# Kernel optimization log

Measured on AMD Instinct MI355X. Metric: run time of the kernel, lower is better.

The kernel has to match this reference:

```python
import jax, jax.numpy as jnp
import numpy as np

N_GENE, N_DRUG, N_CLASS, N_FAM = 100000, 50000, 2000, 5000
D = 64
E_CG, E_CP, E_GF = 2000000, 100000, 200000
N_PAIRS = 100000


def setup_inputs() -> dict:
    key = jax.random.key(0)
    ks = jax.random.split(key, 32)
    nrm = lambda k, s, sc=0.1: jax.random.normal(k, s, jnp.float32) * sc
    ri = lambda k, n, hi: jax.random.randint(k, (n,), 0, hi, jnp.int32)
    inp = {
        "gene_emb": nrm(ks[0], (N_GENE, D)),
        "drug_emb": nrm(ks[1], (N_DRUG, D)),
        "class_emb": nrm(ks[2], (N_CLASS, D)),
        "family_emb": nrm(ks[3], (N_FAM, D)),
        "W_msg": nrm(ks[4], (2, 6, D, D)),
        "b_msg": jnp.zeros((2, 6, D), jnp.float32),
        "W_root": nrm(ks[5], (2, 6, D, D)),
        "Wc1": nrm(ks[6], (2 * D, D)),
        "bc1": jnp.zeros((D,), jnp.float32),
        "Wc2": nrm(ks[7], (D, 4)),
        "bc2": jnp.zeros((4,), jnp.float32),
        "e_cg_src": ri(ks[8], E_CG, N_DRUG), "e_cg_dst": ri(ks[9], E_CG, N_GENE),
        "e_gc_src": ri(ks[10], E_CG, N_GENE), "e_gc_dst": ri(ks[11], E_CG, N_DRUG),
        "e_cp_src": ri(ks[12], E_CP, N_DRUG), "e_cp_dst": ri(ks[13], E_CP, N_CLASS),
        "e_pc_src": ri(ks[14], E_CP, N_CLASS), "e_pc_dst": ri(ks[15], E_CP, N_DRUG),
        "e_gf_src": ri(ks[16], E_GF, N_GENE), "e_gf_dst": ri(ks[17], E_GF, N_FAM),
        "e_fg_src": ri(ks[18], E_GF, N_FAM), "e_fg_dst": ri(ks[19], E_GF, N_GENE),
        "pair_drug": ri(ks[20], N_PAIRS, N_DRUG),
        "pair_gene": ri(ks[21], N_PAIRS, N_GENE),
    }
    return inp


def _sage(x_src, x_dst, src, dst, n_dst, Wm, bm, Wr):
    # PyG SAGEConv(aggr='mean'): lin_l(mean_j x_src[j]) + lin_r(x_dst)
    msg = x_src[src]                                            # [E, D] gather
    agg = jax.ops.segment_sum(msg, dst, num_segments=n_dst)     # [n_dst, D]
    cnt = jax.ops.segment_sum(jnp.ones(src.shape, msg.dtype), dst, num_segments=n_dst)
    mean = agg / jnp.maximum(cnt, 1.0)[:, None]                 # isolated nodes -> 0
    return mean @ Wm + bm + x_dst @ Wr


def reference(gene_emb, drug_emb, class_emb, family_emb, W_msg, b_msg, W_root,
              Wc1, bc1, Wc2, bc2,
              e_cg_src, e_cg_dst, e_gc_src, e_gc_dst, e_cp_src, e_cp_dst,
              e_pc_src, e_pc_dst, e_gf_src, e_gf_dst, e_fg_src, e_fg_dst,
              pair_drug, pair_gene):
    sizes = {"gene": N_GENE, "compound": N_DRUG, "pclass": N_CLASS, "family": N_FAM}
    rels = [  # (src_type, dst_type, src_idx, dst_idx), order matches W_msg relation axis
        ("compound", "gene", e_cg_src, e_cg_dst),
        ("gene", "compound", e_gc_src, e_gc_dst),
        ("compound", "pclass", e_cp_src, e_cp_dst),
        ("pclass", "compound", e_pc_src, e_pc_dst),
        ("gene", "family", e_gf_src, e_gf_dst),
        ("family", "gene", e_fg_src, e_fg_dst),
    ]
    x = {"gene": gene_emb, "compound": drug_emb, "pclass": class_emb, "family": family_emb}
    num_layers = 2
    for l in range(num_layers):
        out = {k: jnp.zeros((sizes[k], D), jnp.float32) for k in sizes}  # HeteroConv aggr='sum'
        for r, (s, d, src, dst) in enumerate(rels):
            out[d] = out[d] + _sage(x[s], x[d], src, dst, sizes[d],
                                    W_msg[l, r], b_msg[l, r], W_root[l, r])
        x = out
        if l < num_layers - 1:
            x = {k: jax.nn.relu(v) for k, v in x.items()}  # dropout = identity (eval)
    h = jnp.concatenate([x["compound"][pair_drug], x["gene"][pair_gene]], axis=-1)  # [N, 2D]
    h = jax.nn.relu(h @ Wc1 + bc1)
    return h @ Wc2 + bc2  # [N, 4]
```

## Files before the change

### kernel.cpp

```cpp
#include <hip/hip_runtime.h>
#include <hip/hip_bf16.h>

#define NG 100000
#define ND 50000
#define NC 2000
#define NF 5000
#define DD 64

#define BSH 9
#define BINW 512
#define NREL 6
#define NB_CG ((NG + BINW - 1) / BINW)
#define NB_GC ((ND + BINW - 1) / BINW)
#define NB_CP ((NC + BINW - 1) / BINW)
#define NB_PC ((ND + BINW - 1) / BINW)
#define NB_GF ((NF + BINW - 1) / BINW)
#define NB_FG ((NG + BINW - 1) / BINW)
#define TOTB (NB_CG + NB_GC + NB_CP + NB_PC + NB_GF + NB_FG)
#define CHUNK 4096

typedef _Float16 h2_t __attribute__((ext_vector_type(2)));
typedef _Float16 half8 __attribute__((ext_vector_type(8)));
typedef float f32x4 __attribute__((ext_vector_type(4)));

__device__ inline uint packh2_rne(float a, float b) {
    h2_t h; h.x = (_Float16)a; h.y = (_Float16)b;
    return __builtin_bit_cast(uint, h);
}
__device__ inline uint packh2(float a, float b) {
    return __builtin_bit_cast(uint, __builtin_amdgcn_cvt_pkrtz(a, b));
}
__device__ inline float2 h2f2(uint u) {
    h2_t h = __builtin_bit_cast(h2_t, u);
    return make_float2((float)h.x, (float)h.y);
}
__device__ inline float fdot2u(uint m, uint w, float acc) {
#if __has_builtin(__builtin_amdgcn_fdot2)
    return __builtin_amdgcn_fdot2(__builtin_bit_cast(h2_t, m),
                                  __builtin_bit_cast(h2_t, w), acc, false);
#else
    float2 a = h2f2(m), b = h2f2(w);
    return acc + a.x * b.x + a.y * b.y;
#endif
}

struct Cvt4 { const float* in[4]; uint* out[4]; int n2[4]; };
struct EdgeJobs {
    const int* src[NREL]; const int* dst[NREL];
    int binbase[NREL]; int E[NREL]; int blk_end[NREL];
};
struct BPackJobs {
    const float* A[6]; const float* B[6]; const float* Ra[6]; const float* Rb[6];
    uint4* out[6]; int nkt[6];
};

struct MegaA {
    EdgeJobs ej; Cvt4 cv; BPackJobs bp;
    const float* Wc1; uint2* pwWc1;
    int hist_blocks, cvt_blocks;
    int* ghist;
};
__global__ __launch_bounds__(256) void megaA_kernel(MegaA a) {
    int b = blockIdx.x;
    if (b < a.hist_blocks) {
        __shared__ int lh[TOTB];
        for (int t = threadIdx.x; t < TOTB; t += 256) lh[t] = 0;
        __syncthreads();
        int j = 0;
        while (b >= a.ej.blk_end[j]) ++j;
        int b0 = j ? a.ej.blk_end[j - 1] : 0;
        int e0 = (b - b0) * CHUNK;
        const int* dst = a.ej.dst[j];
        int E = a.ej.E[j], bb = a.ej.binbase[j];
        for (int t = threadIdx.x; t < CHUNK; t += 256) {
            int e = e0 + t;
            if (e < E) atomicAdd(&lh[bb + (dst[e] >> BSH)], 1);
        }
        __syncthreads();
        for (int t = threadIdx.x; t < TOTB; t += 256)
            if (lh[t]) atomicAdd(&a.ghist[t], lh[t]);
    } else if (b < a.hist_blocks + a.cvt_blocks) {
        int cb = b - a.hist_blocks;
        for (int j = 0; j < 4; ++j) {
            int n2 = a.cv.n2[j];
            const float2* ip = (const float2*)a.cv.in[j];
            uint* op = a.cv.out[j];
            for (int i = cb * 256 + threadIdx.x; i < n2; i += a.cvt_blocks * 256)
                op[i] = packh2_rne(ip[i].x, ip[i].y);
        }
    } else if (b == a.hist_blocks + a.cvt_blocks) {
        const float* A = a.Wc1;
        uint2* o = a.pwWc1;
        for (int t = threadIdx.x; t < 32 * 64; t += 256) {
            int k4 = t >> 6, c = t & 63;
            float v0 = A[(4 * k4 + 0) * 64 + c];
            float v1 = A[(4 * k4 + 1) * 64 + c];
            float v2 = A[(4 * k4 + 2) * 64 + c];
            float v3 = A[(4 * k4 + 3) * 64 + c];
            o[t] = make_uint2(packh2_rne(v0, v1), packh2_rne(v2, v3));
        }
    } else {
        int pj = b - a.hist_blocks - a.cvt_blocks - 1;
        const float* A = a.bp.A[pj];
        const float* B = a.bp.B[pj];
        const float* Ra = a.bp.Ra[pj];
        const float* Rb = a.bp.Rb[pj];
        uint4* o = a.bp.out[pj];
        int n = a.bp.nkt[pj] * 4 * 64;
        for (int t = threadIdx.x; t < n; t += 256) {
            int kt = t >> 8, nt = (t >> 6) & 3, l = t & 63;
            int col = nt * 16 + (l & 15);
            float v[8];
#pragma unroll
            for (int j = 0; j < 8; ++j) {
                int k = kt * 32 + ((l >> 4) << 3) + j;
                int sel = k >> 6, r = k & 63;
                float x;
                if (sel == 0) x = A[r * 64 + col];
                else if (sel == 1 && B) x = B[r * 64 + col];
                else x = Ra[r * 64 + col] + (Rb ? Rb[r * 64 + col] : 0.f);
                v[j] = x;
            }
            o[t] = make_uint4(packh2_rne(v[0], v[1]), packh2_rne(v[2], v[3]),
                              packh2_rne(v[4], v[5]), packh2_rne(v[6], v[7]));
        }
    }
}

__global__ void scanB_kernel(const int* __restrict__ ghist, int* __restrict__ gbinstart,
                             int* __restrict__ gcursor) {
    int lane = threadIdx.x;
    if (lane >= 64) return;
    int carry = 0;
    for (int base = 0; base < TOTB; base += 64) {
        int idx = base + lane;
        int v = (idx < TOTB) ? ghist[idx] : 0;
        int ts = v;
        for (int d = 1; d < 64; d <<= 1) { int t = __shfl_up(ts, d); if (lane >= d) ts += t; }
        int excl = carry + ts - v;
        if (idx < TOTB) { gbinstart[idx] = excl; gcursor[idx] = excl; }
        carry += __shfl(ts, 63);
    }
    if (lane == 0) gbinstart[TOTB] = carry;
}

__global__ __launch_bounds__(256) void scatC_kernel(EdgeJobs ej, int* __restrict__ gcursor,
                                                    int* __restrict__ binned) {
    __shared__ int lh[TOTB], lbase[TOTB];
    for (int t = threadIdx.x; t < TOTB; t += 256) lh[t] = 0;
    __syncthreads();
    int b = blockIdx.x, j = 0;
    while (b >= ej.blk_end[j]) ++j;
    int b0 = j ? ej.blk_end[j - 1] : 0;
    int e0 = (b - b0) * CHUNK;
    const int* dst = ej.dst[j];
    const int* srcp = ej.src[j];
    int E = ej.E[j], bb = ej.binbase[j];
    for (int t = threadIdx.x; t < CHUNK; t += 256) {
        int e = e0 + t;
        if (e < E) atomicAdd(&lh[bb + (dst[e] >> BSH)], 1);
    }
    __syncthreads();
    for (int t = threadIdx.x; t < TOTB; t += 256) {
        int c = lh[t];
        if (c) { lbase[t] = atomicAdd(&gcursor[t], c); lh[t] = 0; }
    }
    __syncthreads();
    for (int t = threadIdx.x; t < CHUNK; t += 256) {
        int e = e0 + t;
        if (e < E) {
            int d = dst[e];
            int bin = bb + (d >> BSH);
            int p = atomicAdd(&lh[bin], 1);
            binned[lbase[bin] + p] = (srcp[e] << BSH) | (d & (BINW - 1));
        }
    }
}

struct BinMeta { int relbase[NREL + 1]; int* off[NREL]; int ndst[NREL]; };
__global__ __launch_bounds__(256) void csrD_kernel(BinMeta bmt, const int* __restrict__ gbinstart,
                                                   const int* __restrict__ binned,
                                                   int* __restrict__ adj) {
    __shared__ int lcnt[BINW], lexc[BINW];
    int b = blockIdx.x, j = 0;
    while (b >= bmt.relbase[j + 1]) ++j;
    int lb = b - bmt.relbase[j];
    int n0 = lb << BSH;
    int nn = bmt.ndst[j] - n0; if (nn > BINW) nn = BINW;
    int es = gbinstart[b], ee = gbinstart[b + 1];
    for (int t = threadIdx.x; t < BINW; t += 256) lcnt[t] = 0;
    __syncthreads();
    for (int t = es + threadIdx.x; t < ee; t += 256)
        atomicAdd(&lcnt[binned[t] & (BINW - 1)], 1);
    __syncthreads();
    if (threadIdx.x < 64) {
        int lane = threadIdx.x, carry = 0;
        for (int base = 0; base < BINW; base += 64) {
            int v = lcnt[base + lane];
            int ts = v;
            for (int d = 1; d < 64; d <<= 1) { int t2 = __shfl_up(ts, d); if (lane >= d) ts += t2; }
            lexc[base + lane] = carry + ts - v;
            carry += __shfl(ts, 63);
        }
    }
    __syncthreads();
    int* off = bmt.off[j];
    for (int t = threadIdx.x; t < nn; t += 256) off[n0 + t] = es + lexc[t];
    if (threadIdx.x == 0 && n0 + nn == bmt.ndst[j]) off[bmt.ndst[j]] = ee;
    for (int t = threadIdx.x; t < BINW; t += 256) lcnt[t] = 0;
    __syncthreads();
    for (int t = es + threadIdx.x; t < ee; t += 256) {
        int v = binned[t];
        int dl = v & (BINW - 1);
        int p = atomicAdd(&lcnt[dl], 1);
        adj[es + lexc[dl] + p] = v >> BSH;
    }
}

__device__ inline void gather2(const int* __restrict__ off, const int* __restrict__ adj,
                               const uint2* __restrict__ xp,
                               int ia, bool hb, int rg, int cq,
                               float4& ma, float4& mb) {
    int a0 = off[ia], a1 = off[ia + 1];
    int b1v = hb ? off[ia + 2] : a1;
    int na = a1 - a0, nb = b1v - a1;
    const int* Ba = adj + a0;
    const int* Bb = adj + a1;
    float4 sa = {0.f, 0.f, 0.f, 0.f}, sb = {0.f, 0.f, 0.f, 0.f};
    int mx = na > nb ? na : nb;
    if (mx <= 8) {
        for (int j = 0; j < mx; j += 4) {
            int e = j + rg;
            if (j < na) {
                int l = na - 1;
                int s0 = Ba[e < l ? e : l];
                uint2 v0 = xp[(long long)s0 * 16 + cq];
                if (e < na) { float2 lo = h2f2(v0.x), hi = h2f2(v0.y); sa.x += lo.x; sa.y += lo.y; sa.z += hi.x; sa.w += hi.y; }
            }
            if (j < nb) {
                int l = nb - 1;
                int s0 = Bb[e < l ? e : l];
                uint2 v0 = xp[(long long)s0 * 16 + cq];
                if (e < nb) { float2 lo = h2f2(v0.x), hi = h2f2(v0.y); sb.x += lo.x; sb.y += lo.y; sb.z += hi.x; sb.w += hi.y; }
            }
        }
    } else {
        for (int j = 0; j < mx; j += 16) {
            int e0 = j + rg, e1 = j + 4 + rg, e2 = j + 8 + rg, e3 = j + 12 + rg;
            if (j < na) {
                int l = na - 1;
                int s0 = Ba[e0 < l ? e0 : l], s1 = Ba[e1 < l ? e1 : l];
                int s2 = Ba[e2 < l ? e2 : l], s3 = Ba[e3 < l ? e3 : l];
                uint2 v0 = xp[(long long)s0 * 16 + cq];
                uint2 v1 = xp[(long long)s1 * 16 + cq];
                uint2 v2 = xp[(long long)s2 * 16 + cq];
                uint2 v3 = xp[(long long)s3 * 16 + cq];
                if (e0 < na) { float2 lo = h2f2(v0.x), hi = h2f2(v0.y); sa.x += lo.x; sa.y += lo.y; sa.z += hi.x; sa.w += hi.y; }
                if (e1 < na) { float2 lo = h2f2(v1.x), hi = h2f2(v1.y); sa.x += lo.x; sa.y += lo.y; sa.z += hi.x; sa.w += hi.y; }
                if (e2 < na) { float2 lo = h2f2(v2.x), hi = h2f2(v2.y); sa.x += lo.x; sa.y += lo.y; sa.z += hi.x; sa.w += hi.y; }
                if (e3 < na) { float2 lo = h2f2(v3.x), hi = h2f2(v3.y); sa.x += lo.x; sa.y += lo.y; sa.z += hi.x; sa.w += hi.y; }
            }
            if (j < nb) {
                int l = nb - 1;
                int s0 = Bb[e0 < l ? e0 : l], s1 = Bb[e1 < l ? e1 : l];
                int s2 = Bb[e2 < l ? e2 : l], s3 = Bb[e3 < l ? e3 : l];
                uint2 v0 = xp[(long long)s0 * 16 + cq];
                uint2 v1 = xp[(long long)s1 * 16 + cq];
                uint2 v2 = xp[(long long)s2 * 16 + cq];
                uint2 v3 = xp[(long long)s3 * 16 + cq];
                if (e0 < nb) { float2 lo = h2f2(v0.x), hi = h2f2(v0.y); sb.x += lo.x; sb.y += lo.y; sb.z += hi.x; sb.w += hi.y; }
                if (e1 < nb) { float2 lo = h2f2(v1.x), hi = h2f2(v1.y); sb.x += lo.x; sb.y += lo.y; sb.z += hi.x; sb.w += hi.y; }
                if (e2 < nb) { float2 lo = h2f2(v2.x), hi = h2f2(v2.y); sb.x += lo.x; sb.y += lo.y; sb.z += hi.x; sb.w += hi.y; }
                if (e3 < nb) { float2 lo = h2f2(v3.x), hi = h2f2(v3.y); sb.x += lo.x; sb.y += lo.y; sb.z += hi.x; sb.w += hi.y; }
            }
        }
    }
    sa.x += __shfl_xor(sa.x, 16); sa.y += __shfl_xor(sa.y, 16);
    sa.z += __shfl_xor(sa.z, 16); sa.w += __shfl_xor(sa.w, 16);
    sa.x += __shfl_xor(sa.x, 32); sa.y += __shfl_xor(sa.y, 32);
    sa.z += __shfl_xor(sa.z, 32); sa.w += __shfl_xor(sa.w, 32);
    sb.x += __shfl_xor(sb.x, 16); sb.y += __shfl_xor(sb.y, 16);
    sb.z += __shfl_xor(sb.z, 16); sb.w += __shfl_xor(sb.w, 16);
    sb.x += __shfl_xor(sb.x, 32); sb.y += __shfl_xor(sb.y, 32);
    sb.z += __shfl_xor(sb.z, 32); sb.w += __shfl_xor(sb.w, 32);
    float inva = 1.f / fmaxf((float)na, 1.f);
    float invb = 1.f / fmaxf((float)nb, 1.f);
    ma.x = sa.x * inva; ma.y = sa.y * inva; ma.z = sa.z * inva; ma.w = sa.w * inva;
    mb.x = sb.x * invb; mb.y = sb.y * invb; mb.z = sb.z * invb; mb.w = sb.w * invb;
}

struct GatherJobs {
    const int* offA[4]; const int* offB[4];
    const uint2* xA[4]; const uint2* xB[4];
    uint2* cat[4]; int cstr[4]; int n[4]; int hasB[4]; int blk_end[4];
};
__global__ __launch_bounds__(256) void gather_kernel(GatherJobs g, const int* __restrict__ adj,
                                                     int njobs) {
    int b = blockIdx.x, j = 0;
    while (b >= g.blk_end[j]) ++j;
    int b0 = j ? g.blk_end[j - 1] : 0;
    int jb = g.blk_end[j] - b0;
    int n = g.n[j], cstr = g.cstr[j], hasB = g.hasB[j];
    const int* offA = g.offA[j];
    const int* offB = g.offB[j];
    const uint2* xA = g.xA[j];
    const uint2* xB = g.xB[j];
    uint2* cat = g.cat[j];
    int tid = threadIdx.x;
    int w = tid >> 6, lane = tid & 63, rg = lane >> 4, cq = lane & 15;
    for (int i0 = (b - b0) * 8; i0 < n; i0 += jb * 8) {
        int ia = i0 + w * 2;
        if (ia >= n) continue;
        int ib = ia + 1;
        bool hb = (ib < n);
        float4 mA0, mA1;
        gather2(offA, adj, xA, ia, hb, rg, cq, mA0, mA1);
        if (rg == 0) {
            cat[(long long)ia * cstr + cq] = make_uint2(packh2(mA0.x, mA0.y), packh2(mA0.z, mA0.w));
            if (hb) cat[(long long)ib * cstr + cq] = make_uint2(packh2(mA1.x, mA1.y), packh2(mA1.z, mA1.w));
        }
        if (hasB) {
            float4 mB0, mB1;
            gather2(offB, adj, xB, ia, hb, rg, cq, mB0, mB1);
            if (rg == 0) {
                cat[(long long)ia * cstr + 16 + cq] = make_uint2(packh2(mB0.x, mB0.y), packh2(mB0.z, mB0.w));
                if (hb) cat[(long long)ib * cstr + 16 + cq] = make_uint2(packh2(mB1.x, mB1.y), packh2(mB1.z, mB1.w));
            }
        }
    }
}

struct ApplyJobs {
    const uint4* cat[4]; const uint4* xr[4]; const uint4* Bimg[4];
    const float* bA[4]; const float* bB[4];
    ushort* out[4];
    int cat_kt[4]; int cstr4[4]; int n[4]; int relu[4]; int blk_end[4];
};
__global__ __launch_bounds__(256) void apply_kernel(ApplyJobs a, int njobs) {
    int b = blockIdx.x, j = 0;
    while (b >= a.blk_end[j]) ++j;
    int b0 = j ? a.blk_end[j - 1] : 0;
    int jb = a.blk_end[j] - b0;
    int n = a.n[j], cat_kt = a.cat_kt[j], cstr4 = a.cstr4[j], relu = a.relu[j];
    int K_kt = cat_kt + 2;
    const uint4* cat = a.cat[j];
    const uint4* xr = a.xr[j];
    const uint4* Bimg = a.Bimg[j];
    const float* bA = a.bA[j];
    const float* bB = a.bB[j];
    ushort* out = a.out[j];
    int tid = threadIdx.x;
    int w = tid >> 6, lane = tid & 63;
    int mrow = lane & 15, koct = lane >> 4;
    int tiles = (n + 15) >> 4;
    for (int t = (b - b0) * 4 + w; t < tiles; t += jb * 4) {
        int m0 = t << 4;
        int row = m0 + mrow;
        if (row > n - 1) row = n - 1;
        f32x4 acc0 = {0.f, 0.f, 0.f, 0.f};
        f32x4 acc1 = {0.f, 0.f, 0.f, 0.f};
        f32x4 acc2 = {0.f, 0.f, 0.f, 0.f};
        f32x4 acc3 = {0.f, 0.f, 0.f, 0.f};
        for (int kt = 0; kt < K_kt; ++kt) {
            uint4 av;
            if (kt < cat_kt) av = cat[(long long)row * cstr4 + kt * 4 + koct];
            else av = xr[(long long)row * 8 + (kt - cat_kt) * 4 + koct];
            half8 af = __builtin_bit_cast(half8, av);
            const uint4* bp = Bimg + kt * 256 + lane;
            half8 b0f = __builtin_bit_cast(half8, bp[0]);
            half8 b1f = __builtin_bit_cast(half8, bp[64]);
            half8 b2f = __builtin_bit_cast(half8, bp[128]);
            half8 b3f = __builtin_bit_cast(half8, bp[192]);
            acc0 = __builtin_amdgcn_mfma_f32_16x16x32_f16(af, b0f, acc0, 0, 0, 0);
            acc1 = __builtin_amdgcn_mfma_f32_16x16x32_f16(af, b1f, acc1, 0, 0, 0);
            acc2 = __builtin_amdgcn_mfma_f32_16x16x32_f16(af, b2f, acc2, 0, 0, 0);
            acc3 = __builtin_amdgcn_mfma_f32_16x16x32_f16(af, b3f, acc3, 0, 0, 0);
        }
        int c = lane & 15, r0 = m0 + (lane >> 4) * 4;
        f32x4 accs[4] = {acc0, acc1, acc2, acc3};
#pragma unroll
        for (int nt = 0; nt < 4; ++nt) {
            int col = nt * 16 + c;
            float bias = bA[col] + (bB ? bB[col] : 0.f);
#pragma unroll
            for (int r = 0; r < 4; ++r) {
                int rw = r0 + r;
                if (rw < n) {
                    float v = accs[nt][r] + bias;
                    if (relu) v = fmaxf(v, 0.f);
                    out[(long long)rw * 64 + col] = __builtin_bit_cast(ushort, (_Float16)v);
                }
            }
        }
    }
}

__global__ __launch_bounds__(256) void classifier_kernel(
        const ushort* __restrict__ xc, const ushort* __restrict__ xg,
        const int* __restrict__ pd, const int* __restrict__ pg,
        const uint2* __restrict__ gW1, const float* __restrict__ bc1,
        const float* __restrict__ Wc2, const float* __restrict__ bc2,
        float* __restrict__ out, int n) {
    __shared__ uint2 sW1[2048];
    __shared__ float sW2[256];
    __shared__ uint2 shp[4][32];
    __shared__ float sh1[4][65];
    int tid = threadIdx.x;
    for (int t = tid; t < 2048; t += 256) sW1[t] = gW1[t];
    if (tid < 256) sW2[tid] = Wc2[tid];
    __syncthreads();
    int lane = tid & 63, sub = tid >> 6;
    float b1 = bc1[lane];
    const uint* xcp = (const uint*)xc;
    const uint* xgp = (const uint*)xg;
    for (int base = blockIdx.x * 4; base < n; base += gridDim.x * 4) {
        int p = base + sub;
        if (p >= n) continue;
        int dp = pd[p], gp = pg[p];
        uint v = (lane < 32) ? xcp[(long long)dp * 32 + lane]
                             : xgp[(long long)gp * 32 + (lane - 32)];
        ((uint*)&shp[sub][0])[lane] = v;
        float acc = b1;
#pragma unroll
        for (int k4 = 0; k4 < 32; ++k4) {
            uint2 wv = sW1[k4 * 64 + lane];
            uint2 mv = shp[sub][k4];
            acc = fdot2u(mv.x, wv.x, acc);
            acc = fdot2u(mv.y, wv.y, acc);
        }
        sh1[sub][lane] = fmaxf(acc, 0.f);
        if (lane < 4) {
            float a2 = bc2[lane];
#pragma unroll 16
            for (int k = 0; k < 64; ++k) a2 += sh1[sub][k] * sW2[k * 4 + lane];
            out[(long long)p * 4 + lane] = a2;
        }
    }
}

extern "C" void kernel_launch(void* const* d_in, const int* in_sizes, int n_in,
                              void* d_out, int out_size, void* d_ws, size_t ws_size,
                              hipStream_t stream) {
    const float* gene = (const float*)d_in[0];
    const float* drug = (const float*)d_in[1];
    const float* pcls = (const float*)d_in[2];
    const float* famb = (const float*)d_in[3];
    const float* Wm   = (const float*)d_in[4];
    const float* bm   = (const float*)d_in[5];
    const float* Wr   = (const float*)d_in[6];
    const float* Wc1  = (const float*)d_in[7];
    const float* bc1  = (const float*)d_in[8];
    const float* Wc2  = (const float*)d_in[9];
    const float* bc2  = (const float*)d_in[10];
    const int* ecg_s = (const int*)d_in[11];
    const int* ecg_d = (const int*)d_in[12];
    const int* egc_s = (const int*)d_in[13];
    const int* egc_d = (const int*)d_in[14];
    const int* ecp_s = (const int*)d_in[15];
    const int* ecp_d = (const int*)d_in[16];
    const int* epc_s = (const int*)d_in[17];
    const int* epc_d = (const int*)d_in[18];
    const int* egf_s = (const int*)d_in[19];
    const int* egf_d = (const int*)d_in[20];
    const int* efg_s = (const int*)d_in[21];
    const int* efg_d = (const int*)d_in[22];
    const int* pair_d = (const int*)d_in[23];
    const int* pair_g = (const int*)d_in[24];
    const int E_CG = in_sizes[11];
    const int E_CP = in_sizes[15];
    const int E_GF = in_sizes[19];
    const int N_PAIRS = in_sizes[23];
    const long long TOT_E = 2LL * E_CG + 2LL * E_CP + 2LL * E_GF;

    ushort* g16   = (ushort*)d_ws;
    ushort* d16   = g16   + (long long)NG * DD;
    ushort* p16   = d16   + (long long)ND * DD;
    ushort* f16b  = p16   + (long long)NC * DD;
    ushort* x1g16 = f16b  + (long long)NF * DD;
    ushort* x1c16 = x1g16 + (long long)NG * DD;
    ushort* x1p16 = x1c16 + (long long)ND * DD;
    ushort* x1f16 = x1p16 + (long long)NC * DD;
    ushort* x2g16 = g16;
    ushort* x2c16 = d16;
    uint2* pwWc1 = (uint2*)(x1f16 + (long long)NF * DD);
    uint4* bimg = (uint4*)(pwWc1 + 2048);
    int* ghist = (int*)(bimg + 6 * 1536);
    int* gbinstart = ghist + TOTB;
    int* gcursor = gbinstart + TOTB + 1;
    int* off_cg = gcursor + TOTB;
    int* off_gc = off_cg + NG + 1;
    int* off_cp = off_gc + ND + 1;
    int* off_pc = off_cp + NC + 1;
    int* off_gf = off_pc + ND + 1;
    int* off_fg = off_gf + NF + 1;
    long long binned_off = (long long)(off_fg + NG + 1 - (int*)d_ws);
    binned_off = (binned_off + 3) & ~3LL;
    int* binned = (int*)d_ws + binned_off;
    int* adj    = binned + TOT_E;
    uint2* cat_c = (uint2*)binned;
    uint2* cat_p = cat_c + (long long)ND * 32;
    uint2* cat_f = cat_p + (long long)NC * 16;
    uint2* cat_g = (uint2*)(adj + TOT_E);

    auto WmLR = [&](int l, int r) { return Wm + (long long)(l * 6 + r) * DD * DD; };
    auto WrLR = [&](int l, int r) { return Wr + (long long)(l * 6 + r) * DD * DD; };
    auto bmLR = [&](int l, int r) { return bm + (long long)(l * 6 + r) * DD; };

    EdgeJobs ej;
    const int* srcs[NREL] = {ecg_s, egc_s, ecp_s, epc_s, egf_s, efg_s};
    const int* dsts[NREL] = {ecg_d, egc_d, ecp_d, epc_d, egf_d, efg_d};
    int Es[NREL] = {E_CG, E_CG, E_CP, E_CP, E_GF, E_GF};
    int bb[NREL] = {0, NB_CG, NB_CG + NB_GC, NB_CG + NB_GC + NB_CP,
                    NB_CG + NB_GC + NB_CP + NB_PC, NB_CG + NB_GC + NB_CP + NB_PC + NB_GF};
    int acc_blocks = 0;
    for (int j = 0; j < NREL; ++j) {
        ej.src[j] = srcs[j]; ej.dst[j] = dsts[j];
        ej.E[j] = Es[j]; ej.binbase[j] = bb[j];
        acc_blocks += (Es[j] + CHUNK - 1) / CHUNK;
        ej.blk_end[j] = acc_blocks;
    }
    const int THIST = acc_blocks;
    const int CVTB = 1024;

    hipMemsetAsync(ghist, 0, TOTB * sizeof(int), stream);
    MegaA ma;
    ma.ej = ej;
    ma.cv.in[0] = gene; ma.cv.out[0] = (uint*)g16;  ma.cv.n2[0] = NG * DD / 2;
    ma.cv.in[1] = drug; ma.cv.out[1] = (uint*)d16;  ma.cv.n2[1] = ND * DD / 2;
    ma.cv.in[2] = pcls; ma.cv.out[2] = (uint*)p16;  ma.cv.n2[2] = NC * DD / 2;
    ma.cv.in[3] = famb; ma.cv.out[3] = (uint*)f16b; ma.cv.n2[3] = NF * DD / 2;
    ma.Wc1 = Wc1; ma.pwWc1 = pwWc1;
    auto setbp = [&](int j, const float* A, const float* B, const float* Ra, const float* Rb, int nkt) {
        ma.bp.A[j] = A; ma.bp.B[j] = B; ma.bp.Ra[j] = Ra; ma.bp.Rb[j] = Rb;
        ma.bp.out[j] = bimg + j * 1536; ma.bp.nkt[j] = nkt;
    };
    setbp(0, WmLR(0, 0), WmLR(0, 5), WrLR(0, 0), WrLR(0, 5), 6);
    setbp(1, WmLR(0, 1), WmLR(0, 3), WrLR(0, 1), WrLR(0, 3), 6);
    setbp(2, WmLR(0, 2), nullptr,    WrLR(0, 2), nullptr,    4);
    setbp(3, WmLR(0, 4), nullptr,    WrLR(0, 4), nullptr,    4);
    setbp(4, WmLR(1, 0), WmLR(1, 5), WrLR(1, 0), WrLR(1, 5), 6);
    setbp(5, WmLR(1, 1), WmLR(1, 3), WrLR(1, 1), WrLR(1, 3), 6);
    ma.hist_blocks = THIST; ma.cvt_blocks = CVTB;
    ma.ghist = ghist;
    megaA_kernel<<<THIST + CVTB + 1 + 6, 256, 0, stream>>>(ma);

    scanB_kernel<<<1, 64, 0, stream>>>(ghist, gbinstart, gcursor);
    scatC_kernel<<<THIST, 256, 0, stream>>>(ej, gcursor, binned);
    BinMeta bmt;
    int rb[NREL + 1] = {0, NB_CG, NB_CG + NB_GC, NB_CG + NB_GC + NB_CP,
                        NB_CG + NB_GC + NB_CP + NB_PC,
                        NB_CG + NB_GC + NB_CP + NB_PC + NB_GF, TOTB};
    int* offs[NREL] = {off_cg, off_gc, off_cp, off_pc, off_gf, off_fg};
    int nds[NREL] = {NG, ND, NC, ND, NF, NG};
    for (int j = 0; j <= NREL; ++j) bmt.relbase[j] = rb[j];
    for (int j = 0; j < NREL; ++j) { bmt.off[j] = offs[j]; bmt.ndst[j] = nds[j]; }
    csrD_kernel<<<TOTB, 256, 0, stream>>>(bmt, gbinstart, binned, adj);

    auto gblk = [](int n) { int b = (n + 7) / 8; return b > 2048 ? 2048 : b; };
    auto ablk = [](int n) { int b = ((n + 15) / 16 + 3) / 4; return b > 1024 ? 1024 : b; };

    {
        GatherJobs g;
        auto setg = [&](int j, const int* oA, const uint2* xA, const int* oB, const uint2* xB,
                        uint2* cat, int cstr, int n, int hb) {
            g.offA[j] = oA; g.offB[j] = oB; g.xA[j] = xA; g.xB[j] = xB;
            g.cat[j] = cat; g.cstr[j] = cstr; g.n[j] = n; g.hasB[j] = hb;
        };
        setg(0, off_cg, (const uint2*)d16, off_fg, (const uint2*)f16b, cat_g, 32, NG, 1);
        setg(1, off_gc, (const uint2*)g16, off_pc, (const uint2*)p16, cat_c, 32, ND, 1);
        setg(2, off_cp, (const uint2*)d16, nullptr, nullptr, cat_p, 16, NC, 0);
        setg(3, off_gf, (const uint2*)g16, nullptr, nullptr, cat_f, 16, NF, 0);
        int acc = 0;
        for (int j = 0; j < 4; ++j) { acc += gblk(g.n[j]); g.blk_end[j] = acc; }
        gather_kernel<<<acc, 256, 0, stream>>>(g, adj, 4);

        ApplyJobs ap;
        auto seta = [&](int j, const uint2* cat, int ckt, int cstr4, const ushort* xr,
                        const uint4* Bi, const float* biA, const float* biB,
                        ushort* out, int n, int relu) {
            ap.cat[j] = (const uint4*)cat; ap.cat_kt[j] = ckt; ap.cstr4[j] = cstr4;
            ap.xr[j] = (const uint4*)xr; ap.Bimg[j] = Bi; ap.bA[j] = biA; ap.bB[j] = biB;
            ap.out[j] = out; ap.n[j] = n; ap.relu[j] = relu;
        };
        seta(0, cat_g, 4, 16, g16,  bimg + 0 * 1536, bmLR(0, 0), bmLR(0, 5), x1g16, NG, 1);
        seta(1, cat_c, 4, 16, d16,  bimg + 1 * 1536, bmLR(0, 1), bmLR(0, 3), x1c16, ND, 1);
        seta(2, cat_p, 2, 8,  p16,  bimg + 2 * 1536, bmLR(0, 2), nullptr,    x1p16, NC, 1);
        seta(3, cat_f, 2, 8,  f16b, bimg + 3 * 1536, bmLR(0, 4), nullptr,    x1f16, NF, 1);
        int acc2 = 0;
        for (int j = 0; j < 4; ++j) { acc2 += ablk(ap.n[j]); ap.blk_end[j] = acc2; }
        apply_kernel<<<acc2, 256, 0, stream>>>(ap, 4);
    }

    {
        GatherJobs g;
        g.offA[0] = off_cg; g.offB[0] = off_fg;
        g.xA[0] = (const uint2*)x1c16; g.xB[0] = (const uint2*)x1f16;
        g.cat[0] = cat_g; g.cstr[0] = 32; g.n[0] = NG; g.hasB[0] = 1;
        g.offA[1] = off_gc; g.offB[1] = off_pc;
        g.xA[1] = (const uint2*)x1g16; g.xB[1] = (const uint2*)x1p16;
        g.cat[1] = cat_c; g.cstr[1] = 32; g.n[1] = ND; g.hasB[1] = 1;
        for (int j = 2; j < 4; ++j) { g.offA[j] = nullptr; g.offB[j] = nullptr; g.xA[j] = nullptr; g.xB[j] = nullptr; g.cat[j] = nullptr; g.cstr[j] = 16; g.n[j] = 0; g.hasB[j] = 0; }
        int acc = gblk(NG); g.blk_end[0] = acc; acc += gblk(ND); g.blk_end[1] = acc;
        g.blk_end[2] = acc; g.blk_end[3] = acc;
        gather_kernel<<<acc, 256, 0, stream>>>(g, adj, 2);

        ApplyJobs ap;
        ap.cat[0] = (const uint4*)cat_g; ap.cat_kt[0] = 4; ap.cstr4[0] = 16;
        ap.xr[0] = (const uint4*)x1g16; ap.Bimg[0] = bimg + 4 * 1536;
        ap.bA[0] = bmLR(1, 0); ap.bB[0] = bmLR(1, 5);
        ap.out[0] = x2g16; ap.n[0] = NG; ap.relu[0] = 0;
        ap.cat[1] = (const uint4*)cat_c; ap.cat_kt[1] = 4; ap.cstr4[1] = 16;
        ap.xr[1] = (const uint4*)x1c16; ap.Bimg[1] = bimg + 5 * 1536;
        ap.bA[1] = bmLR(1, 1); ap.bB[1] = bmLR(1, 3);
        ap.out[1] = x2c16; ap.n[1] = ND; ap.relu[1] = 0;
        for (int j = 2; j < 4; ++j) { ap.cat[j] = nullptr; ap.xr[j] = nullptr; ap.Bimg[j] = nullptr; ap.bA[j] = nullptr; ap.bB[j] = nullptr; ap.out[j] = nullptr; ap.n[j] = 0; ap.relu[j] = 0; ap.cat_kt[j] = 2; ap.cstr4[j] = 8; }
        int acc2 = ablk(NG); ap.blk_end[0] = acc2; acc2 += ablk(ND); ap.blk_end[1] = acc2;
        ap.blk_end[2] = acc2; ap.blk_end[3] = acc2;
        apply_kernel<<<acc2, 256, 0, stream>>>(ap, 2);
    }

    int cblocks = (N_PAIRS + 3) / 4;
    if (cblocks > 2048) cblocks = 2048;
    classifier_kernel<<<cblocks, 256, 0, stream>>>(x2c16, x2g16, pair_d, pair_g,
                                                   pwWc1, bc1, Wc2, bc2,
                                                   (float*)d_out, N_PAIRS);
}
```

Baseline: 473.4 us.

## Restructure gather into per-relation jobs with 16-byte fp16 loads and packed-half accumulation

Replaces the paired-relation gather with six independent per-relation jobs. Each job gets a block count proportional to its edge count and writes its own column half of the concat buffer. Each lane now loads 16 bytes (half8) per row instead of 8 bytes and accumulates in packed fp16 rather than fp32. Low-degree relations use a one-node-per-8-lanes mode so short neighbour lists are not spread across a whole wave. The intent is fewer load instructions, better bandwidth use and better load balance. The cost is reduced accumulation precision: fp16 sums over high-degree nodes may lose accuracy or overflow.

```diff
diff --git a/kernel.cpp b/kernel.cpp
--- a/kernel.cpp
+++ b/kernel.cpp
@@ -26,9 +26,6 @@
 __device__ inline uint packh2_rne(float a, float b) {
     h2_t h; h.x = (_Float16)a; h.y = (_Float16)b;
     return __builtin_bit_cast(uint, h);
-}
-__device__ inline uint packh2(float a, float b) {
-    return __builtin_bit_cast(uint, __builtin_amdgcn_cvt_pkrtz(a, b));
 }
 __device__ inline float2 h2f2(uint u) {
     h2_t h = __builtin_bit_cast(h2_t, u);
@@ -217,115 +214,74 @@
     }
 }
 
-__device__ inline void gather2(const int* __restrict__ off, const int* __restrict__ adj,
-                               const uint2* __restrict__ xp,
-                               int ia, bool hb, int rg, int cq,
-                               float4& ma, float4& mb) {
-    int a0 = off[ia], a1 = off[ia + 1];
-    int b1v = hb ? off[ia + 2] : a1;
-    int na = a1 - a0, nb = b1v - a1;
-    const int* Ba = adj + a0;
-    const int* Bb = adj + a1;
-    float4 sa = {0.f, 0.f, 0.f, 0.f}, sb = {0.f, 0.f, 0.f, 0.f};
-    int mx = na > nb ? na : nb;
-    if (mx <= 8) {
-        for (int j = 0; j < mx; j += 4) {
-            int e = j + rg;
-            if (j < na) {
-                int l = na - 1;
-                int s0 = Ba[e < l ? e : l];
-                uint2 v0 = xp[(long long)s0 * 16 + cq];
-                if (e < na) { float2 lo = h2f2(v0.x), hi = h2f2(v0.y); sa.x += lo.x; sa.y += lo.y; sa.z += hi.x; sa.w += hi.y; }
-            }
-            if (j < nb) {
-                int l = nb - 1;
-                int s0 = Bb[e < l ? e : l];
-                uint2 v0 = xp[(long long)s0 * 16 + cq];
-                if (e < nb) { float2 lo = h2f2(v0.x), hi = h2f2(v0.y); sb.x += lo.x; sb.y += lo.y; sb.z += hi.x; sb.w += hi.y; }
-            }
-        }
-    } else {
-        for (int j = 0; j < mx; j += 16) {
-            int e0 = j + rg, e1 = j + 4 + rg, e2 = j + 8 + rg, e3 = j + 12 + rg;
-            if (j < na) {
-                int l = na - 1;
-                int s0 = Ba[e0 < l ? e0 : l], s1 = Ba[e1 < l ? e1 : l];
-                int s2 = Ba[e2 < l ? e2 : l], s3 = Ba[e3 < l ? e3 : l];
-                uint2 v0 = xp[(long long)s0 * 16 + cq];
-                uint2 v1 = xp[(long long)s1 * 16 + cq];
-                uint2 v2 = xp[(long long)s2 * 16 + cq];
-                uint2 v3 = xp[(long long)s3 * 16 + cq];
-                if (e0 < na) { float2 lo = h2f2(v0.x), hi = h2f2(v0.y); sa.x += lo.x; sa.y += lo.y; sa.z += hi.x; sa.w += hi.y; }
-                if (e1 < na) { float2 lo = h2f2(v1.x), hi = h2f2(v1.y); sa.x += lo.x; sa.y += lo.y; sa.z += hi.x; sa.w += hi.y; }
-                if (e2 < na) { float2 lo = h2f2(v2.x), hi = h2f2(v2.y); sa.x += lo.x; sa.y += lo.y; sa.z += hi.x; sa.w += hi.y; }
-                if (e3 < na) { float2 lo = h2f2(v3.x), hi = h2f2(v3.y); sa.x += lo.x; sa.y += lo.y; sa.z += hi.x; sa.w += hi.y; }
-            }
-            if (j < nb) {
-                int l = nb - 1;
-                int s0 = Bb[e0 < l ? e0 : l], s1 = Bb[e1 < l ? e1 : l];
-                int s2 = Bb[e2 < l ? e2 : l], s3 = Bb[e3 < l ? e3 : l];
-                uint2 v0 = xp[(long long)s0 * 16 + cq];
-                uint2 v1 = xp[(long long)s1 * 16 + cq];
-                uint2 v2 = xp[(long long)s2 * 16 + cq];
-                uint2 v3 = xp[(long long)s3 * 16 + cq];
-                if (e0 < nb) { float2 lo = h2f2(v0.x), hi = h2f2(v0.y); sb.x += lo.x; sb.y += lo.y; sb.z += hi.x; sb.w += hi.y; }
-                if (e1 < nb) { float2 lo = h2f2(v1.x), hi = h2f2(v1.y); sb.x += lo.x; sb.y += lo.y; sb.z += hi.x; sb.w += hi.y; }
-                if (e2 < nb) { float2 lo = h2f2(v2.x), hi = h2f2(v2.y); sb.x += lo.x; sb.y += lo.y; sb.z += hi.x; sb.w += hi.y; }
-                if (e3 < nb) { float2 lo = h2f2(v3.x), hi = h2f2(v3.y); sb.x += lo.x; sb.y += lo.y; sb.z += hi.x; sb.w += hi.y; }
-            }
-        }
-    }
-    sa.x += __shfl_xor(sa.x, 16); sa.y += __shfl_xor(sa.y, 16);
-    sa.z += __shfl_xor(sa.z, 16); sa.w += __shfl_xor(sa.w, 16);
-    sa.x += __shfl_xor(sa.x, 32); sa.y += __shfl_xor(sa.y, 32);
-    sa.z += __shfl_xor(sa.z, 32); sa.w += __shfl_xor(sa.w, 32);
-    sb.x += __shfl_xor(sb.x, 16); sb.y += __shfl_xor(sb.y, 16);
-    sb.z += __shfl_xor(sb.z, 16); sb.w += __shfl_xor(sb.w, 16);
-    sb.x += __shfl_xor(sb.x, 32); sb.y += __shfl_xor(sb.y, 32);
-    sb.z += __shfl_xor(sb.z, 32); sb.w += __shfl_xor(sb.w, 32);
-    float inva = 1.f / fmaxf((float)na, 1.f);
-    float invb = 1.f / fmaxf((float)nb, 1.f);
-    ma.x = sa.x * inva; ma.y = sa.y * inva; ma.z = sa.z * inva; ma.w = sa.w * inva;
-    mb.x = sb.x * invb; mb.y = sb.y * invb; mb.z = sb.z * invb; mb.w = sb.w * invb;
-}
-
-struct GatherJobs {
-    const int* offA[4]; const int* offB[4];
-    const uint2* xA[4]; const uint2* xB[4];
-    uint2* cat[4]; int cstr[4]; int n[4]; int hasB[4]; int blk_end[4];
-};
-__global__ __launch_bounds__(256) void gather_kernel(GatherJobs g, const int* __restrict__ adj,
-                                                     int njobs) {
+struct GJob { const int* off; const uint4* x; uint4* cat; int cstr, colbase, n, mode; };
+struct GatherJobs { GJob jb[6]; int blk_end[6]; };
+
+__global__ __launch_bounds__(256) void gather_kernel(GatherJobs g, const int* __restrict__ adj) {
     int b = blockIdx.x, j = 0;
     while (b >= g.blk_end[j]) ++j;
     int b0 = j ? g.blk_end[j - 1] : 0;
-    int jb = g.blk_end[j] - b0;
-    int n = g.n[j], cstr = g.cstr[j], hasB = g.hasB[j];
-    const int* offA = g.offA[j];
-    const int* offB = g.offB[j];
-    const uint2* xA = g.xA[j];
-    const uint2* xB = g.xB[j];
-    uint2* cat = g.cat[j];
-    int tid = threadIdx.x;
-    int w = tid >> 6, lane = tid & 63, rg = lane >> 4, cq = lane & 15;
-    for (int i0 = (b - b0) * 8; i0 < n; i0 += jb * 8) {
-        int ia = i0 + w * 2;
-        if (ia >= n) continue;
-        int ib = ia + 1;
-        bool hb = (ib < n);
-        float4 mA0, mA1;
-        gather2(offA, adj, xA, ia, hb, rg, cq, mA0, mA1);
-        if (rg == 0) {
-            cat[(long long)ia * cstr + cq] = make_uint2(packh2(mA0.x, mA0.y), packh2(mA0.z, mA0.w));
-            if (hb) cat[(long long)ib * cstr + cq] = make_uint2(packh2(mA1.x, mA1.y), packh2(mA1.z, mA1.w));
-        }
-        if (hasB) {
-            float4 mB0, mB1;
-            gather2(offB, adj, xB, ia, hb, rg, cq, mB0, mB1);
-            if (rg == 0) {
-                cat[(long long)ia * cstr + 16 + cq] = make_uint2(packh2(mB0.x, mB0.y), packh2(mB0.z, mB0.w));
-                if (hb) cat[(long long)ib * cstr + 16 + cq] = make_uint2(packh2(mB1.x, mB1.y), packh2(mB1.z, mB1.w));
+    int nbk = g.blk_end[j] - b0;
+    GJob jb = g.jb[j];
+    int tid = threadIdx.x, w = tid >> 6, lane = tid & 63;
+    int cq = lane & 7, rg = lane >> 3;
+    if (jb.mode == 0) {
+        int side = rg >> 2, sub = rg & 3;
+        int npair = (jb.n + 1) >> 1;
+        for (int p = (b - b0) * 4 + w; p < npair; p += nbk * 4) {
+            int ia = p * 2;
+            bool hb = (ia + 1 < jb.n);
+            int a0 = jb.off[ia], a1 = jb.off[ia + 1];
+            int b1 = hb ? jb.off[ia + 2] : a1;
+            int cnt = side ? (b1 - a1) : (a1 - a0);
+            const int* base = adj + (side ? a1 : a0);
+            half8 acc = {0, 0, 0, 0, 0, 0, 0, 0};
+            int full = cnt & ~3;
+            for (int e = sub; e < full; e += 4) {
+                int idx = base[e];
+                acc += *(const half8*)(jb.x + (long long)idx * 8 + cq);
             }
+            int e = full + sub;
+            if (e < cnt) {
+                int idx = base[e];
+                acc += *(const half8*)(jb.x + (long long)idx * 8 + cq);
+            }
+            uint4 u = __builtin_bit_cast(uint4, acc), o;
+            o.x = __shfl_xor((int)u.x, 8); o.y = __shfl_xor((int)u.y, 8);
+            o.z = __shfl_xor((int)u.z, 8); o.w = __shfl_xor((int)u.w, 8);
+            acc += __builtin_bit_cast(half8, o);
+            u = __builtin_bit_cast(uint4, acc);
+            o.x = __shfl_xor((int)u.x, 16); o.y = __shfl_xor((int)u.y, 16);
+            o.z = __shfl_xor((int)u.z, 16); o.w = __shfl_xor((int)u.w, 16);
+            acc += __builtin_bit_cast(half8, o);
+            float invf = 1.f / fmaxf((float)cnt, 1.f);
+            _Float16 ih = (_Float16)invf;
+            half8 iv = {ih, ih, ih, ih, ih, ih, ih, ih};
+            acc *= iv;
+            if (sub == 0 && (side == 0 || hb)) {
+                int node = ia + side;
+                jb.cat[(long long)node * jb.cstr + jb.colbase + cq] =
+                    __builtin_bit_cast(uint4, acc);
+            }
+        }
+    } else {
+        for (int gp = (b - b0) * 4 + w; gp * 8 < jb.n; gp += nbk * 4) {
+            int node = gp * 8 + rg;
+            int nc = node < jb.n ? node : jb.n - 1;
+            int o0 = jb.off[nc], o1 = jb.off[nc + 1];
+            int cnt = (node < jb.n) ? (o1 - o0) : 0;
+            half8 acc = {0, 0, 0, 0, 0, 0, 0, 0};
+            for (int t = 0; t < cnt; ++t) {
+                int idx = adj[o0 + t];
+                acc += *(const half8*)(jb.x + (long long)idx * 8 + cq);
+            }
+            float invf = 1.f / fmaxf((float)cnt, 1.f);
+            _Float16 ih = (_Float16)invf;
+            half8 iv = {ih, ih, ih, ih, ih, ih, ih, ih};
+            acc *= iv;
+            if (node < jb.n)
+                jb.cat[(long long)node * jb.cstr + jb.colbase + cq] =
+                    __builtin_bit_cast(uint4, acc);
         }
     }
 }
@@ -497,10 +453,10 @@
     binned_off = (binned_off + 3) & ~3LL;
     int* binned = (int*)d_ws + binned_off;
     int* adj    = binned + TOT_E;
-    uint2* cat_c = (uint2*)binned;
-    uint2* cat_p = cat_c + (long long)ND * 32;
-    uint2* cat_f = cat_p + (long long)NC * 16;
-    uint2* cat_g = (uint2*)(adj + TOT_E);
+    uint4* cat_c = (uint4*)binned;
+    uint4* cat_p = cat_c + (long long)ND * 16;
+    uint4* cat_f = cat_p + (long long)NC * 8;
+    uint4* cat_g = (uint4*)(adj + TOT_E);
 
     auto WmLR = [&](int l, int r) { return Wm + (long long)(l * 6 + r) * DD * DD; };
     auto WrLR = [&](int l, int r) { return Wr + (long long)(l * 6 + r) * DD * DD; };
@@ -556,29 +512,31 @@
     for (int j = 0; j < NREL; ++j) { bmt.off[j] = offs[j]; bmt.ndst[j] = nds[j]; }
     csrD_kernel<<<TOTB, 256, 0, stream>>>(bmt, gbinstart, binned, adj);
 
-    auto gblk = [](int n) { int b = (n + 7) / 8; return b > 2048 ? 2048 : b; };
     auto ablk = [](int n) { int b = ((n + 15) / 16 + 3) / 4; return b > 1024 ? 1024 : b; };
+    auto gb = [](int E) { int b = E / 1024; if (b < 8) b = 8; if (b > 2048) b = 2048; return b; };
 
     {
         GatherJobs g;
-        auto setg = [&](int j, const int* oA, const uint2* xA, const int* oB, const uint2* xB,
-                        uint2* cat, int cstr, int n, int hb) {
-            g.offA[j] = oA; g.offB[j] = oB; g.xA[j] = xA; g.xB[j] = xB;
-            g.cat[j] = cat; g.cstr[j] = cstr; g.n[j] = n; g.hasB[j] = hb;
+        int acc = 0;
+        auto setg = [&](int j, const int* off, const ushort* x, uint4* cat,
+                        int cstr, int colbase, int n, int mode, int E) {
+            g.jb[j].off = off; g.jb[j].x = (const uint4*)x; g.jb[j].cat = cat;
+            g.jb[j].cstr = cstr; g.jb[j].colbase = colbase; g.jb[j].n = n; g.jb[j].mode = mode;
+            acc += gb(E); g.blk_end[j] = acc;
         };
-        setg(0, off_cg, (const uint2*)d16, off_fg, (const uint2*)f16b, cat_g, 32, NG, 1);
-        setg(1, off_gc, (const uint2*)g16, off_pc, (const uint2*)p16, cat_c, 32, ND, 1);
-        setg(2, off_cp, (const uint2*)d16, nullptr, nullptr, cat_p, 16, NC, 0);
-        setg(3, off_gf, (const uint2*)g16, nullptr, nullptr, cat_f, 16, NF, 0);
-        int acc = 0;
-        for (int j = 0; j < 4; ++j) { acc += gblk(g.n[j]); g.blk_end[j] = acc; }
-        gather_kernel<<<acc, 256, 0, stream>>>(g, adj, 4);
+        setg(0, off_cg, d16,  cat_g, 16, 0, NG, 0, E_CG);
+        setg(1, off_fg, f16b, cat_g, 16, 8, NG, 1, E_GF);
+        setg(2, off_gc, g16,  cat_c, 16, 0, ND, 0, E_CG);
+        setg(3, off_pc, p16,  cat_c, 16, 8, ND, 1, E_CP);
+        setg(4, off_cp, d16,  cat_p, 8, 0, NC, 0, E_CP);
+        setg(5, off_gf, g16,  cat_f, 8, 0, NF, 0, E_GF);
+        gather_kernel<<<acc, 256, 0, stream>>>(g, adj);
 
         ApplyJobs ap;
-        auto seta = [&](int j, const uint2* cat, int ckt, int cstr4, const ushort* xr,
+        auto seta = [&](int j, const uint4* cat, int ckt, int cstr4, const ushort* xr,
                         const uint4* Bi, const float* biA, const float* biB,
                         ushort* out, int n, int relu) {
-            ap.cat[j] = (const uint4*)cat; ap.cat_kt[j] = ckt; ap.cstr4[j] = cstr4;
+            ap.cat[j] = cat; ap.cat_kt[j] = ckt; ap.cstr4[j] = cstr4;
             ap.xr[j] = (const uint4*)xr; ap.Bimg[j] = Bi; ap.bA[j] = biA; ap.bB[j] = biB;
             ap.out[j] = out; ap.n[j] = n; ap.relu[j] = relu;
         };
@@ -593,23 +551,27 @@
 
     {
         GatherJobs g;
-        g.offA[0] = off_cg; g.offB[0] = off_fg;
-        g.xA[0] = (const uint2*)x1c16; g.xB[0] = (const uint2*)x1f16;
-        g.cat[0] = cat_g; g.cstr[0] = 32; g.n[0] = NG; g.hasB[0] = 1;
-        g.offA[1] = off_gc; g.offB[1] = off_pc;
-        g.xA[1] = (const uint2*)x1g16; g.xB[1] = (const uint2*)x1p16;
-        g.cat[1] = cat_c; g.cstr[1] = 32; g.n[1] = ND; g.hasB[1] = 1;
-        for (int j = 2; j < 4; ++j) { g.offA[j] = nullptr; g.offB[j] = nullptr; g.xA[j] = nullptr; g.xB[j] = nullptr; g.cat[j] = nullptr; g.cstr[j] = 16; g.n[j] = 0; g.hasB[j] = 0; }
-        int acc = gblk(NG); g.blk_end[0] = acc; acc += gblk(ND); g.blk_end[1] = acc;
-        g.blk_end[2] = acc; g.blk_end[3] = acc;
-        gather_kernel<<<acc, 256, 0, stream>>>(g, adj, 2);
+        int acc = 0;
+        auto setg = [&](int j, const int* off, const ushort* x, uint4* cat,
+                        int cstr, int colbase, int n, int mode, int E) {
+            g.jb[j].off = off; g.jb[j].x = (const uint4*)x; g.jb[j].cat = cat;
+            g.jb[j].cstr = cstr; g.jb[j].colbase = colbase; g.jb[j].n = n; g.jb[j].mode = mode;
+            acc += gb(E); g.blk_end[j] = acc;
+        };
+        setg(0, off_cg, x1c16, cat_g, 16, 0, NG, 0, E_CG);
+        setg(1, off_fg, x1f16, cat_g, 16, 8, NG, 1, E_GF);
+        setg(2, off_gc, x1g16, cat_c, 16, 0, ND, 0, E_CG);
+        setg(3, off_pc, x1p16, cat_c, 16, 8, ND, 1, E_CP);
+        g.jb[4] = g.jb[3]; g.jb[4].n = 0; g.blk_end[4] = acc;
+        g.jb[5] = g.jb[3]; g.jb[5].n = 0; g.blk_end[5] = acc;
+        gather_kernel<<<acc, 256, 0, stream>>>(g, adj);
 
         ApplyJobs ap;
-        ap.cat[0] = (const uint4*)cat_g; ap.cat_kt[0] = 4; ap.cstr4[0] = 16;
+        ap.cat[0] = cat_g; ap.cat_kt[0] = 4; ap.cstr4[0] = 16;
         ap.xr[0] = (const uint4*)x1g16; ap.Bimg[0] = bimg + 4 * 1536;
         ap.bA[0] = bmLR(1, 0); ap.bB[0] = bmLR(1, 5);
         ap.out[0] = x2g16; ap.n[0] = NG; ap.relu[0] = 0;
-        ap.cat[1] = (const uint4*)cat_c; ap.cat_kt[1] = 4; ap.cstr4[1] = 16;
+        ap.cat[1] = cat_c; ap.cat_kt[1] = 4; ap.cstr4[1] = 16;
         ap.xr[1] = (const uint4*)x1c16; ap.Bimg[1] = bimg + 5 * 1536;
         ap.bA[1] = bmLR(1, 1); ap.bB[1] = bmLR(1, 3);
         ap.out[1] = x2c16; ap.n[1] = ND; ap.relu[1] = 0;
```

Result: slower. 488.4 us (+3.2%).
